# Performance work log

Measured on AMD Instinct MI355X. Metric: run time of the kernel, lower is better.

## Reference

```python
import jax, jax.numpy as jnp
import numpy as np

B, N, DIN, DMID, DOUT, E = 64, 5000, 64, 128, 32, 80000


def setup_inputs() -> dict:
    key = jax.random.key(0)
    ks = jax.random.split(key, 12)
    p = lambda k, shape: jax.random.normal(k, shape, jnp.float32) * 0.05
    return {
        "x": jax.random.normal(ks[0], (B, N, DIN), jnp.float32),
        "edge_index": jax.random.randint(ks[1], (2, E), 0, N),
        "prev_hidden_state": jax.random.normal(ks[2], (B, N, DMID), jnp.float32),
        # GCNConv weights/biases for gates z, r, h
        "Wg_z": p(ks[3], (DIN, DMID)), "bg_z": jnp.zeros((DMID,), jnp.float32),
        "Wg_r": p(ks[4], (DIN, DMID)), "bg_r": jnp.zeros((DMID,), jnp.float32),
        "Wg_h": p(ks[5], (DIN, DMID)), "bg_h": jnp.zeros((DMID,), jnp.float32),
        # gate Linear layers on concat([conv_out, H]) -> DMID
        "Wl_z": p(ks[6], (2 * DMID, DMID)), "bl_z": jnp.zeros((DMID,), jnp.float32),
        "Wl_r": p(ks[7], (2 * DMID, DMID)), "bl_r": jnp.zeros((DMID,), jnp.float32),
        "Wl_h": p(ks[8], (2 * DMID, DMID)), "bl_h": jnp.zeros((DMID,), jnp.float32),
        # final output Linear
        "W_out": p(ks[9], (DMID, DOUT)), "b_out": jnp.zeros((DOUT,), jnp.float32),
    }


def reference(x, edge_index, prev_hidden_state,
              Wg_z, bg_z, Wg_r, bg_r, Wg_h, bg_h,
              Wl_z, bl_z, Wl_r, bl_r, Wl_h, bl_h,
              W_out, b_out):
    # GCN symmetric normalization with self-loops (pyg gcn_norm, improved=False)
    row, col = edge_index[0], edge_index[1]
    loop = jnp.arange(N)
    src = jnp.concatenate([row, loop])          # [E+N]
    dst = jnp.concatenate([col, loop])          # [E+N]
    ew = jnp.ones((E + N,), x.dtype)
    deg = jnp.zeros((N,), x.dtype).at[dst].add(ew)
    dis = jnp.where(deg > 0, jax.lax.rsqrt(jnp.maximum(deg, 1e-12)), 0.0)
    norm = dis[src] * ew * dis[dst]             # [E+N]

    def gcn(w, b):
        xw = jnp.einsum('bnd,de->bne', x, w)            # [B,N,DMID]
        msg = xw[:, src, :] * norm[None, :, None]       # gather + weight
        out = jnp.zeros((B, N, w.shape[1]), x.dtype).at[:, dst, :].add(msg)
        return out + b

    H = prev_hidden_state
    Z = jax.nn.sigmoid(jnp.concatenate([gcn(Wg_z, bg_z), H], -1) @ Wl_z + bl_z)
    R = jax.nn.sigmoid(jnp.concatenate([gcn(Wg_r, bg_r), H], -1) @ Wl_r + bl_r)
    Ht = jnp.tanh(jnp.concatenate([gcn(Wg_h, bg_h), H * R], -1) @ Wl_h + bl_h)
    H_new = Z * H + (1.0 - Z) * Ht                      # [B,N,DMID]

    y = jnp.mean(H_new, axis=1)                         # MeanAggregation over nodes
    y = jax.nn.relu(y) @ W_out + b_out                  # [B,DOUT]
    return (y, H_new)
```

## Files before the change

### kernel.cpp

```cpp
#include <hip/hip_runtime.h>
#include <cmath>

namespace {

constexpr int B = 64, N = 5000, DIN = 64, DMID = 128, DOUT = 32, E = 80000;
constexpr int NT = (N + 63) / 64;

typedef unsigned short u16;
typedef __attribute__((ext_vector_type(8))) short short8;
typedef __attribute__((ext_vector_type(4))) float floatx4;

#define MFMA16(a, b, c) __builtin_amdgcn_mfma_f32_16x16x32_bf16((a), (b), (c), 0, 0, 0)

__device__ __forceinline__ u16 f2bf(float f) {
  union { float f; unsigned u; } v; v.f = f;
  unsigned r = v.u + 0x7FFFu + ((v.u >> 16) & 1u);
  return (u16)(r >> 16);
}
__device__ __forceinline__ float bf2f(u16 s) {
  union { unsigned u; float f; } v; v.u = ((unsigned)s) << 16;
  return v.f;
}
__device__ __forceinline__ float sigmoid_fast(float x) {
  return __builtin_amdgcn_rcpf(1.f + __expf(-x));
}
__device__ __forceinline__ float tanh_fast(float x) {
  return fmaf(2.f, __builtin_amdgcn_rcpf(1.f + __expf(-2.f * x)), -1.f);
}


__global__ void zero_kernel(int* counts, int* fill) {
  int i = blockIdx.x * 256 + threadIdx.x;
  if (i < N) { counts[i] = 0; fill[i] = 0; }
}

__global__ void count_kernel(const int* __restrict__ ei, int* counts) {
  int e = blockIdx.x * 256 + threadIdx.x;
  if (e < E) atomicAdd(&counts[ei[E + e]], 1);
}

__global__ void scan_kernel(const int* __restrict__ counts, int* rowptr, float* dis) {
  __shared__ int sdata[1024];
  const int tid = threadIdx.x;
  constexpr int CH = (N + 1023) / 1024;
  int local[CH];
  int s = 0;
  for (int i = 0; i < CH; i++) {
    int idx = tid * CH + i;
    int c = (idx < N) ? counts[idx] : 0;
    local[i] = s;
    s += c;
  }
  sdata[tid] = s;
  __syncthreads();
  for (int off = 1; off < 1024; off <<= 1) {
    int v = (tid >= off) ? sdata[tid - off] : 0;
    __syncthreads();
    sdata[tid] += v;
    __syncthreads();
  }
  int prev = (tid > 0) ? sdata[tid - 1] : 0;
  for (int i = 0; i < CH; i++) {
    int idx = tid * CH + i;
    if (idx < N) {
      rowptr[idx] = prev + local[i];
      dis[idx] = rsqrtf((float)(counts[idx] + 1));
    }
  }
  if (tid == 1023) rowptr[N] = sdata[1023];
}

__global__ void fill_kernel(const int* __restrict__ ei, const int* __restrict__ rowptr,
                            const float* __restrict__ dis, int* fill,
                            int* csr_src, float* csr_w) {
  int e = blockIdx.x * 256 + threadIdx.x;
  if (e >= E) return;
  int r = ei[e], c = ei[E + e];
  int pos = rowptr[c] + atomicAdd(&fill[c], 1);
  csr_src[pos] = r;
  csr_w[pos] = dis[r] * dis[c];
}


__global__ void pack_kernel(const float* Wgz, const float* Wgr, const float* Wgh,
                            const float* Wlz, const float* Wlr, const float* Wlh,
                            const float* bgz, const float* bgr, const float* bgh,
                            const float* blz, const float* blr, const float* blh,
                            u16* wcB, u16* whB, float* bcAll) {
  int t = blockIdx.x * 256 + threadIdx.x;
  const float* Wg[3] = {Wgz, Wgr, Wgh};
  const float* Wl[3] = {Wlz, Wlr, Wlh};
  const float* bg[3] = {bgz, bgr, bgh};
  const float* bl[3] = {blz, blr, blh};
  if (t < 48 * 64) {
    int chunk = t >> 6, lane = t & 63;
    int q = lane >> 4, lm = lane & 15;
    int g = chunk >> 4, rem = chunk & 15, kt = rem >> 3, nt = rem & 7;
    int n = nt * 16 + lm;
#pragma unroll
    for (int jj = 0; jj < 8; jj++) {
      int k = kt * 32 + q * 8 + jj;
      float acc = 0.f;
      for (int j = 0; j < DMID; j++)
        acc = fmaf(Wg[g][k * DMID + j], Wl[g][j * DMID + n], acc);
      wcB[(size_t)(chunk * 64 + lane) * 8 + jj] = f2bf(acc);
    }
  } else if (t < 48 * 64 + 96 * 64) {
    int t2 = t - 48 * 64;
    int chunk = t2 >> 6, lane = t2 & 63;
    int q = lane >> 4, lm = lane & 15;
    int g = chunk >> 5, rem = chunk & 31, kt = rem >> 3, nt = rem & 7;
    int n = nt * 16 + lm;
#pragma unroll
    for (int jj = 0; jj < 8; jj++) {
      int k = kt * 32 + q * 8 + jj;
      whB[(size_t)t2 * 8 + jj] = f2bf(Wl[g][(DMID + k) * DMID + n]);
    }
  } else {
    int t3 = t - 48 * 64 - 96 * 64;
    if (t3 < 384) {
      int g = t3 >> 7, n = t3 & 127;
      float acc = bl[g][n];
      for (int j = 0; j < DMID; j++)
        acc = fmaf(bg[g][j], Wl[g][j * DMID + n], acc);
      bcAll[t3] = acc;
    }
  }
}


__global__ __launch_bounds__(256) void agg_kernel(
    const float* __restrict__ x, const int* __restrict__ rowptr,
    const int* __restrict__ csr_src, const float* __restrict__ csr_w,
    const float* __restrict__ dis, u16* __restrict__ xs) {
  constexpr int G = B * N / 16;
  const int bid = blockIdx.x;
  const int nb = (bid & 7) * (G >> 3) + (bid >> 3);
  const int sub = threadIdx.x >> 4;
  const int l16 = threadIdx.x & 15;
  const int unit = nb * 16 + sub;
  const int b = unit / N;
  const int n = unit - b * N;
  const float* xb = x + (size_t)b * N * DIN;
  const float d = dis[n];
  float4 v = *(const float4*)(xb + (size_t)n * DIN + l16 * 4);
  const float sw = d * d;
  float ax = v.x * sw, ay = v.y * sw, az = v.z * sw, aw = v.w * sw;
  const int s1 = rowptr[n + 1];
  int p = rowptr[n];
  for (; p + 2 <= s1; p += 2) {
    int i0 = csr_src[p], i1 = csr_src[p + 1];
    float w0 = csr_w[p], w1 = csr_w[p + 1];
    float4 a0 = *(const float4*)(xb + (size_t)i0 * DIN + l16 * 4);
    float4 a1 = *(const float4*)(xb + (size_t)i1 * DIN + l16 * 4);
    ax = fmaf(a0.x, w0, ax); ay = fmaf(a0.y, w0, ay);
    az = fmaf(a0.z, w0, az); aw = fmaf(a0.w, w0, aw);
    ax = fmaf(a1.x, w1, ax); ay = fmaf(a1.y, w1, ay);
    az = fmaf(a1.z, w1, az); aw = fmaf(a1.w, w1, aw);
  }
  if (p < s1) {
    int i0 = csr_src[p];
    float w0 = csr_w[p];
    float4 a0 = *(const float4*)(xb + (size_t)i0 * DIN + l16 * 4);
    ax = fmaf(a0.x, w0, ax); ay = fmaf(a0.y, w0, ay);
    az = fmaf(a0.z, w0, az); aw = fmaf(a0.w, w0, aw);
  }
  uint2 o;
  o.x = (unsigned)f2bf(ax) | ((unsigned)f2bf(ay) << 16);
  o.y = (unsigned)f2bf(az) | ((unsigned)f2bf(aw) << 16);
  *(uint2*)(xs + (size_t)unit * DIN + l16 * 4) = o;
}


constexpr int SH = 136;
constexpr int SX = 72;

__global__ __launch_bounds__(256, 6) void fused_mfma(
    const u16* __restrict__ xs, const float* __restrict__ H,
    const u16* __restrict__ wcB, const u16* __restrict__ whB,
    const float* __restrict__ bcAll,
    float* __restrict__ hnew, float* __restrict__ partials) {
  __shared__ u16 H_s[64 * SH];
  __shared__ u16 XS_s[64 * SX];
  __shared__ float lds_sum[DMID];

  const int tid = threadIdx.x;
  const int b = blockIdx.y;
  const int n0 = blockIdx.x * 64;
  const int lane = tid & 63, w = tid >> 6;
  const int q = lane >> 4, lm = lane & 15;
  const int w16 = w * 16;

  if (tid < DMID) lds_sum[tid] = 0.f;

#pragma unroll
  for (int i = 0; i < 2; i++) {
    int idx = i * 256 + tid;
    int row = idx >> 3, seg = idx & 7;
    uint4 v = make_uint4(0u, 0u, 0u, 0u);
    if (n0 + row < N) v = *(const uint4*)(xs + ((size_t)b * N + n0 + row) * DIN + seg * 8);
    *(uint4*)&XS_s[row * SX + seg * 8] = v;
  }
#pragma unroll
  for (int i = 0; i < 8; i++) {
    int idx = i * 256 + tid;
    int row = idx >> 5, seg = idx & 31;
    float4 v = make_float4(0.f, 0.f, 0.f, 0.f);
    if (n0 + row < N) v = *(const float4*)(H + ((size_t)b * N + n0 + row) * DMID + seg * 4);
    uint2 p;
    p.x = (unsigned)f2bf(v.x) | ((unsigned)f2bf(v.y) << 16);
    p.y = (unsigned)f2bf(v.z) | ((unsigned)f2bf(v.w) << 16);
    *(uint2*)&H_s[row * SH + seg * 4] = p;
  }
  __syncthreads();

  short8 ax[2], ah[4];
#pragma unroll
  for (int kt = 0; kt < 2; kt++)
    ax[kt] = *(const short8*)&XS_s[(w16 + lm) * SX + kt * 32 + q * 8];
#pragma unroll
  for (int kt = 0; kt < 4; kt++)
    ah[kt] = *(const short8*)&H_s[(w16 + lm) * SH + kt * 32 + q * 8];

  floatx4 racc[8];
#pragma unroll
  for (int nt = 0; nt < 8; nt++) {
    floatx4 a = {0.f, 0.f, 0.f, 0.f};
#pragma unroll
    for (int kt = 0; kt < 2; kt++)
      a = MFMA16(ax[kt], *(const short8*)(wcB + (size_t)((16 + kt * 8 + nt) * 64 + lane) * 8), a);
#pragma unroll
    for (int kt = 0; kt < 4; kt++)
      a = MFMA16(ah[kt], *(const short8*)(whB + (size_t)((32 + kt * 8 + nt) * 64 + lane) * 8), a);
    float bias = bcAll[128 + nt * 16 + lm];
#pragma unroll
    for (int r = 0; r < 4; r++) racc[nt][r] = a[r] + bias;
  }

#pragma unroll
  for (int nt = 0; nt < 8; nt++)
#pragma unroll
    for (int r = 0; r < 4; r++) {
      int row = w16 + q * 4 + r, col = nt * 16 + lm;
      float h = bf2f(H_s[row * SH + col]);
      float rg = sigmoid_fast(racc[nt][r]);
      H_s[row * SH + col] = f2bf(h * rg);
      racc[nt][r] = h;
    }
  __syncthreads();

  short8 ahr[4];
#pragma unroll
  for (int kt = 0; kt < 4; kt++)
    ahr[kt] = *(const short8*)&H_s[(w16 + lm) * SH + kt * 32 + q * 8];

#pragma unroll
  for (int nt = 0; nt < 8; nt++) {
    floatx4 za = {0.f, 0.f, 0.f, 0.f}, ha = {0.f, 0.f, 0.f, 0.f};
#pragma unroll
    for (int kt = 0; kt < 2; kt++) {
      za = MFMA16(ax[kt], *(const short8*)(wcB + (size_t)((0 + kt * 8 + nt) * 64 + lane) * 8), za);
      ha = MFMA16(ax[kt], *(const short8*)(wcB + (size_t)((32 + kt * 8 + nt) * 64 + lane) * 8), ha);
    }
#pragma unroll
    for (int kt = 0; kt < 4; kt++) {
      za = MFMA16(ah[kt], *(const short8*)(whB + (size_t)((0 + kt * 8 + nt) * 64 + lane) * 8), za);
      ha = MFMA16(ahr[kt], *(const short8*)(whB + (size_t)((64 + kt * 8 + nt) * 64 + lane) * 8), ha);
    }
    float zb = bcAll[nt * 16 + lm], hb = bcAll[256 + nt * 16 + lm];
    float colsum = 0.f;
#pragma unroll
    for (int r = 0; r < 4; r++) {
      int row = w16 + q * 4 + r;
      bool valid = (n0 + row) < N;
      float z = sigmoid_fast(za[r] + zb);
      float ht = tanh_fast(ha[r] + hb);
      float h = racc[nt][r];
      float hn = fmaf(z, h - ht, ht);
      if (valid) {
        hnew[((size_t)b * N + n0 + row) * DMID + nt * 16 + lm] = hn;
        colsum += hn;
      }
    }
    colsum += __shfl_xor(colsum, 16);
    colsum += __shfl_xor(colsum, 32);
    if (lane < 16) atomicAdd(&lds_sum[nt * 16 + lane], colsum);
  }

  __syncthreads();
  if (tid < DMID)
    partials[((size_t)b * NT + blockIdx.x) * DMID + tid] = lds_sum[tid];
}


__global__ void out_kernel(const float* __restrict__ partials, const float* __restrict__ Wout,
                           const float* __restrict__ bout, float* __restrict__ y) {
  const int b = blockIdx.x;
  const int c = threadIdx.x;
  __shared__ float m[DMID];
  float acc = 0.f;
  for (int t = 0; t < NT; t++)
    acc += partials[((size_t)b * NT + t) * DMID + c];
  m[c] = fmaxf(acc * (1.f / (float)N), 0.f);
  __syncthreads();
  if (c < DOUT) {
    float a2 = bout[c];
    for (int jj = 0; jj < DMID; jj++)
      a2 = fmaf(m[jj], Wout[jj * DOUT + c], a2);
    y[b * DOUT + c] = a2;
  }
}

}

extern "C" void kernel_launch(void* const* d_in, const int* in_sizes, int n_in,
                              void* d_out, int out_size, void* d_ws, size_t ws_size,
                              hipStream_t stream) {
  const float* x = (const float*)d_in[0];
  const int* ei = (const int*)d_in[1];
  const float* H = (const float*)d_in[2];
  const float* Wgz = (const float*)d_in[3];
  const float* bgz = (const float*)d_in[4];
  const float* Wgr = (const float*)d_in[5];
  const float* bgr = (const float*)d_in[6];
  const float* Wgh = (const float*)d_in[7];
  const float* bgh = (const float*)d_in[8];
  const float* Wlz = (const float*)d_in[9];
  const float* blz = (const float*)d_in[10];
  const float* Wlr = (const float*)d_in[11];
  const float* blr = (const float*)d_in[12];
  const float* Wlh = (const float*)d_in[13];
  const float* blh = (const float*)d_in[14];
  const float* Wout = (const float*)d_in[15];
  const float* bout = (const float*)d_in[16];

  float* y = (float*)d_out;
  float* hnew = (float*)d_out + (size_t)B * DOUT;

  char* p = (char*)d_ws;
  auto carve = [&](size_t bytes) {
    char* q = p;
    p += (bytes + 255) & ~size_t(255);
    return q;
  };
  int* counts = (int*)carve((size_t)N * 4);
  int* rowptr = (int*)carve((size_t)(N + 1) * 4);
  int* fill = (int*)carve((size_t)N * 4);
  int* csr_src = (int*)carve((size_t)E * 4);
  float* csr_w = (float*)carve((size_t)E * 4);
  float* dis = (float*)carve((size_t)N * 4);
  u16* wcB = (u16*)carve((size_t)48 * 64 * 8 * 2);
  u16* whB = (u16*)carve((size_t)96 * 64 * 8 * 2);
  float* bcAll = (float*)carve((size_t)384 * 4);
  float* partials = (float*)carve((size_t)B * NT * DMID * 4);
  u16* xs = (u16*)carve((size_t)B * N * DIN * 2);

  zero_kernel<<<(N + 255) / 256, 256, 0, stream>>>(counts, fill);
  pack_kernel<<<38, 256, 0, stream>>>(Wgz, Wgr, Wgh, Wlz, Wlr, Wlh,
                                      bgz, bgr, bgh, blz, blr, blh,
                                      wcB, whB, bcAll);
  count_kernel<<<(E + 255) / 256, 256, 0, stream>>>(ei, counts);
  scan_kernel<<<1, 1024, 0, stream>>>(counts, rowptr, dis);
  fill_kernel<<<(E + 255) / 256, 256, 0, stream>>>(ei, rowptr, dis, fill, csr_src, csr_w);
  agg_kernel<<<B * N / 16, 256, 0, stream>>>(x, rowptr, csr_src, csr_w, dis, xs);
  fused_mfma<<<dim3(NT, B), 256, 0, stream>>>(xs, H, wcB, whB, bcAll, hnew, partials);
  out_kernel<<<B, DMID, 0, stream>>>(partials, Wout, bout, y);
}
```

Baseline: 854.7 us.

## Make fused GRU kernel wave-local, drop block barriers and LDS staging

In the fused MFMA kernel, each wave now loads only its own 16 rows of H into shared memory and reads its X operand straight from global memory. This removes the XS staging buffer and all __syncthreads calls. The shared-memory atomic column sum is replaced by per-wave partial writes, so out_kernel reduces four times as many partials. The graph-setup path also reuses the counts array as the fill counter: scan re-zeroes it and a memset replaces zero_kernel. Launch bounds drop from 6 to 4 blocks per CU, which gives more registers but lowers the occupancy target.

```diff
diff --git a/kernel.cpp b/kernel.cpp
--- a/kernel.cpp
+++ b/kernel.cpp
@@ -29,25 +29,21 @@
 }
 
 
-__global__ void zero_kernel(int* counts, int* fill) {
-  int i = blockIdx.x * 256 + threadIdx.x;
-  if (i < N) { counts[i] = 0; fill[i] = 0; }
-}
-
 __global__ void count_kernel(const int* __restrict__ ei, int* counts) {
   int e = blockIdx.x * 256 + threadIdx.x;
   if (e < E) atomicAdd(&counts[ei[E + e]], 1);
 }
 
-__global__ void scan_kernel(const int* __restrict__ counts, int* rowptr, float* dis) {
+__global__ void scan_kernel(int* counts, int* rowptr, float* dis) {
   __shared__ int sdata[1024];
   const int tid = threadIdx.x;
   constexpr int CH = (N + 1023) / 1024;
-  int local[CH];
+  int local[CH], cnt[CH];
   int s = 0;
   for (int i = 0; i < CH; i++) {
     int idx = tid * CH + i;
     int c = (idx < N) ? counts[idx] : 0;
+    cnt[i] = c;
     local[i] = s;
     s += c;
   }
@@ -64,19 +60,20 @@
     int idx = tid * CH + i;
     if (idx < N) {
       rowptr[idx] = prev + local[i];
-      dis[idx] = rsqrtf((float)(counts[idx] + 1));
+      dis[idx] = rsqrtf((float)(cnt[i] + 1));
+      counts[idx] = 0;
     }
   }
   if (tid == 1023) rowptr[N] = sdata[1023];
 }
 
 __global__ void fill_kernel(const int* __restrict__ ei, const int* __restrict__ rowptr,
-                            const float* __restrict__ dis, int* fill,
+                            const float* __restrict__ dis, int* counts,
                             int* csr_src, float* csr_w) {
   int e = blockIdx.x * 256 + threadIdx.x;
   if (e >= E) return;
   int r = ei[e], c = ei[E + e];
-  int pos = rowptr[c] + atomicAdd(&fill[c], 1);
+  int pos = rowptr[c] + atomicAdd(&counts[c], 1);
   csr_src[pos] = r;
   csr_w[pos] = dis[r] * dis[c];
 }
@@ -173,16 +170,13 @@
 
 
 constexpr int SH = 136;
-constexpr int SX = 72;
-
-__global__ __launch_bounds__(256, 6) void fused_mfma(
+
+__global__ __launch_bounds__(256, 4) void fused_mfma(
     const u16* __restrict__ xs, const float* __restrict__ H,
     const u16* __restrict__ wcB, const u16* __restrict__ whB,
     const float* __restrict__ bcAll,
     float* __restrict__ hnew, float* __restrict__ partials) {
   __shared__ u16 H_s[64 * SH];
-  __shared__ u16 XS_s[64 * SX];
-  __shared__ float lds_sum[DMID];
 
   const int tid = threadIdx.x;
   const int b = blockIdx.y;
@@ -191,20 +185,11 @@
   const int q = lane >> 4, lm = lane & 15;
   const int w16 = w * 16;
 
-  if (tid < DMID) lds_sum[tid] = 0.f;
-
-#pragma unroll
-  for (int i = 0; i < 2; i++) {
-    int idx = i * 256 + tid;
-    int row = idx >> 3, seg = idx & 7;
-    uint4 v = make_uint4(0u, 0u, 0u, 0u);
-    if (n0 + row < N) v = *(const uint4*)(xs + ((size_t)b * N + n0 + row) * DIN + seg * 8);
-    *(uint4*)&XS_s[row * SX + seg * 8] = v;
-  }
-#pragma unroll
-  for (int i = 0; i < 8; i++) {
-    int idx = i * 256 + tid;
-    int row = idx >> 5, seg = idx & 31;
+#pragma unroll
+  for (int j = 0; j < 8; j++) {
+    int idx = j * 64 + lane;
+    int rl = idx >> 5, seg = idx & 31;
+    int row = w16 + rl;
     float4 v = make_float4(0.f, 0.f, 0.f, 0.f);
     if (n0 + row < N) v = *(const float4*)(H + ((size_t)b * N + n0 + row) * DMID + seg * 4);
     uint2 p;
@@ -212,12 +197,19 @@
     p.y = (unsigned)f2bf(v.z) | ((unsigned)f2bf(v.w) << 16);
     *(uint2*)&H_s[row * SH + seg * 4] = p;
   }
-  __syncthreads();
-
-  short8 ax[2], ah[4];
-#pragma unroll
-  for (int kt = 0; kt < 2; kt++)
-    ax[kt] = *(const short8*)&XS_s[(w16 + lm) * SX + kt * 32 + q * 8];
+
+  const int an = n0 + w16 + lm;
+  short8 ax[2];
+  if (an < N) {
+    const u16* xrow = xs + ((size_t)b * N + an) * DIN;
+    ax[0] = *(const short8*)(xrow + q * 8);
+    ax[1] = *(const short8*)(xrow + 32 + q * 8);
+  } else {
+    ax[0] = short8{0, 0, 0, 0, 0, 0, 0, 0};
+    ax[1] = short8{0, 0, 0, 0, 0, 0, 0, 0};
+  }
+
+  short8 ah[4];
 #pragma unroll
   for (int kt = 0; kt < 4; kt++)
     ah[kt] = *(const short8*)&H_s[(w16 + lm) * SH + kt * 32 + q * 8];
@@ -247,7 +239,6 @@
       H_s[row * SH + col] = f2bf(h * rg);
       racc[nt][r] = h;
     }
-  __syncthreads();
 
   short8 ahr[4];
 #pragma unroll
@@ -284,12 +275,9 @@
     }
     colsum += __shfl_xor(colsum, 16);
     colsum += __shfl_xor(colsum, 32);
-    if (lane < 16) atomicAdd(&lds_sum[nt * 16 + lane], colsum);
-  }
-
-  __syncthreads();
-  if (tid < DMID)
-    partials[((size_t)b * NT + blockIdx.x) * DMID + tid] = lds_sum[tid];
+    if (lane < 16)
+      partials[(((size_t)b * NT + blockIdx.x) * 4 + w) * DMID + nt * 16 + lane] = colsum;
+  }
 }
 
 
@@ -299,8 +287,8 @@
   const int c = threadIdx.x;
   __shared__ float m[DMID];
   float acc = 0.f;
-  for (int t = 0; t < NT; t++)
-    acc += partials[((size_t)b * NT + t) * DMID + c];
+  for (int t = 0; t < NT * 4; t++)
+    acc += partials[((size_t)b * NT * 4 + t) * DMID + c];
   m[c] = fmaxf(acc * (1.f / (float)N), 0.f);
   __syncthreads();
   if (c < DOUT) {
@@ -345,23 +333,22 @@
   };
   int* counts = (int*)carve((size_t)N * 4);
   int* rowptr = (int*)carve((size_t)(N + 1) * 4);
-  int* fill = (int*)carve((size_t)N * 4);
   int* csr_src = (int*)carve((size_t)E * 4);
   float* csr_w = (float*)carve((size_t)E * 4);
   float* dis = (float*)carve((size_t)N * 4);
   u16* wcB = (u16*)carve((size_t)48 * 64 * 8 * 2);
   u16* whB = (u16*)carve((size_t)96 * 64 * 8 * 2);
   float* bcAll = (float*)carve((size_t)384 * 4);
-  float* partials = (float*)carve((size_t)B * NT * DMID * 4);
+  float* partials = (float*)carve((size_t)B * NT * 4 * DMID * 4);
   u16* xs = (u16*)carve((size_t)B * N * DIN * 2);
 
-  zero_kernel<<<(N + 255) / 256, 256, 0, stream>>>(counts, fill);
+  hipMemsetAsync(counts, 0, (size_t)N * 4, stream);
   pack_kernel<<<38, 256, 0, stream>>>(Wgz, Wgr, Wgh, Wlz, Wlr, Wlh,
                                       bgz, bgr, bgh, blz, blr, blh,
                                       wcB, whB, bcAll);
   count_kernel<<<(E + 255) / 256, 256, 0, stream>>>(ei, counts);
   scan_kernel<<<1, 1024, 0, stream>>>(counts, rowptr, dis);
-  fill_kernel<<<(E + 255) / 256, 256, 0, stream>>>(ei, rowptr, dis, fill, csr_src, csr_w);
+  fill_kernel<<<(E + 255) / 256, 256, 0, stream>>>(ei, rowptr, dis, counts, csr_src, csr_w);
   agg_kernel<<<B * N / 16, 256, 0, stream>>>(x, rowptr, csr_src, csr_w, dis, xs);
   fused_mfma<<<dim3(NT, B), 256, 0, stream>>>(xs, H, wcB, whB, bcAll, hnew, partials);
   out_kernel<<<B, DMID, 0, stream>>>(partials, Wout, bout, y);
```

New measurement: 715.0 us. 16.4% less time.
